# Optimization experiments

Measured on AMD Instinct MI355X. Metric: run time of the kernel, lower is better.

## Reference

```python
import jax, jax.numpy as jnp
import numpy as np

B, T, X, H, Z, G, Y = 4096, 32, 256, 256, 256, 128, 2


def _xavier(key, fan_in, fan_out):
    lim = float(np.sqrt(6.0 / (fan_in + fan_out)))
    return jax.random.uniform(key, (fan_in, fan_out), jnp.float32, -lim, lim)


def setup_inputs() -> dict:
    key = jax.random.key(0)
    ks = jax.random.split(key, 18)
    return {
        "x": jax.random.normal(ks[0], (B, T, X), jnp.float32),
        "y_ph": jax.random.uniform(ks[1], (B, T, Y), jnp.float32),
        "T_ph": jax.random.randint(ks[2], (B,), 1, T + 1),  # 1..T valid days
        "h0": jnp.tanh(jax.random.normal(ks[3], (B, H), jnp.float32)),   # tanh(randn) init state
        "z0": jnp.tanh(jax.random.normal(ks[4], (B, Z), jnp.float32)),
        "eps": jax.random.normal(ks[5], (T, B, Z), jnp.float32),          # reparam noise per step
        # gate / candidate nets: fan_in = x + h + z
        "Wr": _xavier(ks[6], X + H + Z, H), "br": jnp.zeros((H,), jnp.float32),
        "Wu": _xavier(ks[7], X + H + Z, H), "bu": jnp.zeros((H,), jnp.float32),
        "Wh": _xavier(ks[8], X + H + Z, H), "bh": jnp.zeros((H,), jnp.float32),
        # prior latent net: fan_in = x + h
        "Wzp": _xavier(ks[9], X + H, Z), "bzp": jnp.zeros((Z,), jnp.float32),
        "Wpm": _xavier(ks[10], Z, Z), "bpm": jnp.zeros((Z,), jnp.float32),
        "Wps": _xavier(ks[11], Z, Z), "bps": jnp.zeros((Z,), jnp.float32),
        # posterior latent net: fan_in = x + h + y
        "Wzq": _xavier(ks[12], X + H + Y, Z), "bzq": jnp.zeros((Z,), jnp.float32),
        "Wqm": _xavier(ks[13], Z, Z), "bqm": jnp.zeros((Z,), jnp.float32),
        "Wqs": _xavier(ks[14], Z, Z), "bqs": jnp.zeros((Z,), jnp.float32),
        # output nets
        "Wg": _xavier(ks[15], X + H + Z, G), "bg": jnp.zeros((G,), jnp.float32),
        "Wy": _xavier(ks[16], G, Y), "by": jnp.zeros((Y,), jnp.float32),
    }


def reference(x, y_ph, T_ph, h0, z0, eps,
              Wr, br, Wu, bu, Wh, bh,
              Wzp, bzp, Wpm, bpm, Wps, bps,
              Wzq, bzq, Wqm, bqm, Wqs, bqs,
              Wg, bg, Wy, by):
    x_t = jnp.transpose(x, (1, 0, 2))     # [T, B, X]
    y_t = jnp.transpose(y_ph, (1, 0, 2))  # [T, B, Y]

    def step(carry, inp):
        h_prev, z_prev = carry
        xt, yt, et = inp
        ga = jnp.concatenate([xt, h_prev, z_prev], axis=-1)
        r = jax.nn.sigmoid(ga @ Wr + br)
        u = jax.nn.sigmoid(ga @ Wu + bu)
        ha = jnp.concatenate([xt, r * h_prev, z_prev], axis=-1)
        h_tilde = jnp.tanh(ha @ Wh + bh)
        h = (1.0 - u) * h_prev + u * h_tilde
        # prior p(z_t | x_t, h_t): z_prior = mean (is_prior=True)
        hzp = jnp.tanh(jnp.concatenate([xt, h], axis=-1) @ Wzp + bzp)
        mu_p = hzp @ Wpm + bpm
        sd_p = jnp.sqrt(jnp.exp(hzp @ Wps + bps))
        z_prior = mu_p
        # posterior q(z_t | x_t, h_t, y_t): reparameterized sample
        hzq = jnp.tanh(jnp.concatenate([xt, h, yt], axis=-1) @ Wzq + bzq)
        mu_q = hzq @ Wqm + bqm
        sd_q = jnp.sqrt(jnp.exp(hzq @ Wqs + bqs))
        z_post = mu_q + sd_q * et
        # KL(q || p) for diagonal Normals
        kl = jnp.log(sd_p / sd_q) + (sd_q ** 2 + (mu_q - mu_p) ** 2) / (2.0 * sd_p ** 2) - 0.5
        return (h, z_post), (h, z_post, z_prior, kl)

    (_, _), (h_s, z_post, z_prior, kl) = jax.lax.scan(step, (h0, z0), (x_t, y_t, eps))
    h_s = jnp.transpose(h_s, (1, 0, 2))      # [B, T, H]
    z_post = jnp.transpose(z_post, (1, 0, 2))
    kl = jnp.transpose(kl, (1, 0, 2)).sum(axis=-1)  # [B, T]

    g = jnp.tanh(jnp.concatenate([x, h_s, z_post], axis=-1) @ Wg + bg)  # [B, T, G]
    y = jax.nn.softmax(g @ Wy + by, axis=-1)                             # [B, T, Y]
    g_T = g[jnp.arange(x.shape[0]), T_ph - 1]                            # [B, G] (training, daily_att)
    return (y, kl, g_T)
```

## Files before the change

### kernel.cpp

```cpp
#include <hip/hip_runtime.h>

typedef unsigned short u16;
typedef unsigned int u32;
typedef __attribute__((ext_vector_type(8))) short short8;
typedef __attribute__((ext_vector_type(4))) float float4v;
typedef __attribute__((ext_vector_type(2))) float float2v;

#define B_SZ 4096
#define T_SZ 32
#define XD 256
#define HD 256
#define ZD 256
#define GD 128
#define YD 2

#define BM 64
#define NW 16

#define W1_OFF 0
#define W2_OFF 393216
#define W3_OFF 589824
#define W4_OFF 868352
#define WG_OFF 1130496
#define WTOT   1228800

#define YTOT  (B_SZ*T_SZ*YD)
#define KLTOT (B_SZ*T_SZ)

#define UST 264

__device__ __forceinline__ u16 f2bf(float f) {
    u32 u = __float_as_uint(f);
    u32 r = (u + 0x7fffu + ((u >> 16) & 1u)) >> 16;
    return (u16)r;
}
__device__ __forceinline__ float bf2f(u16 h) {
    return __uint_as_float(((u32)h) << 16);
}
__device__ __forceinline__ float tanh_f(float x) {
    float e = __expf(2.f * x);
    return 1.f - 2.f / (e + 1.f);
}
__device__ __forceinline__ float sigm_f(float x) {
    return 1.f / (1.f + __expf(-x));
}

__device__ __forceinline__ int aga_off(int r, int k) {
    return (((r >> 4) * 24 + (k >> 5)) << 9) + ((((k >> 3) & 3) * 16 + (r & 15)) << 3) + (k & 7);
}
__device__ __forceinline__ int a3_off(int r, int k) {
    return (((r >> 4) * 8 + (k >> 5)) << 9) + ((((k >> 3) & 3) * 16 + (r & 15)) << 3) + (k & 7);
}

#define MFMA(a, b, c) __builtin_amdgcn_mfma_f32_16x16x32_bf16(a, b, c, 0, 0, 0)

__global__ void prep_weights(const float* __restrict__ Wr, const float* __restrict__ Wu,
                             const float* __restrict__ Wh, const float* __restrict__ Wzp,
                             const float* __restrict__ Wzq, const float* __restrict__ Wpm,
                             const float* __restrict__ Wps, const float* __restrict__ Wqm,
                             const float* __restrict__ Wqs, const float* __restrict__ Wg,
                             u16* __restrict__ wts)
{
    int o = blockIdx.x * 256 + threadIdx.x;
    if (o >= WTOT) return;
    int mat, w, KT;
    if (o < W2_OFF)      { mat = 0; w = o;          KT = 24; }
    else if (o < W3_OFF) { mat = 1; w = o - W2_OFF; KT = 24; }
    else if (o < W4_OFF) { mat = 2; w = o - W3_OFF; KT = 17; }
    else if (o < WG_OFF) { mat = 3; w = o - W4_OFF; KT = 8;  }
    else                 { mat = 4; w = o - WG_OFF; KT = 24; }
    int nt  = w / (KT * 512);
    int rem = w - nt * (KT * 512);
    int kt  = rem >> 9;
    int q   = rem & 511;
    int lane = q >> 3, j = q & 7;
    int n = (nt << 4) | (lane & 15);
    int k = (kt << 5) + ((lane >> 4) << 3) + j;
    float v = 0.f;
    switch (mat) {
        case 0: v = (n < 256) ? Wr[k * 256 + n] : Wu[k * 256 + (n - 256)]; break;
        case 1: v = Wh[k * 256 + n]; break;
        case 2: v = (n < 256) ? (k < 512 ? Wzp[k * 256 + n] : 0.f)
                              : (k < 514 ? Wzq[k * 256 + (n - 256)] : 0.f); break;
        case 3: { int sel = n >> 8; int nn = n & 255;
                  const float* s = (sel == 0) ? Wpm : (sel == 1) ? Wps : (sel == 2) ? Wqm : Wqs;
                  v = s[k * 256 + nn]; } break;
        default: v = Wg[k * 128 + n]; break;
    }
    wts[o] = f2bf(v);
}

__global__ __launch_bounds__(1024, 4) void vrnn_all(
    const float* __restrict__ x,   const float* __restrict__ y_ph,
    const int*   __restrict__ Tph, const float* __restrict__ h0,
    const float* __restrict__ z0,  const float* __restrict__ eps,
    const float* __restrict__ br,  const float* __restrict__ bu,
    const float* __restrict__ bh,  const float* __restrict__ bzp,
    const float* __restrict__ bpm, const float* __restrict__ bps,
    const float* __restrict__ bzq, const float* __restrict__ bqm,
    const float* __restrict__ bqs, const float* __restrict__ bg,
    const float* __restrict__ by,  const float* __restrict__ Wy,
    const u16*   __restrict__ wts, float* __restrict__ out)
{
    __shared__ __align__(16) u16   a_ga[96 * 512];
    __shared__ __align__(16) u16   a3u[16896];
    __shared__ float part[8 * BM * 2];
    __shared__ float kl_acc[BM];
    __shared__ int   tph_s[BM];

    const int tid  = threadIdx.x;
    const int wv   = tid >> 6;
    const int lane = tid & 63;
    const int quad = lane >> 4;
    const int l15  = lane & 15;
    const int b0   = blockIdx.x * BM;

    const int c10 = wv * 32 + l15;
    const float bs1_0 = (c10 < 256) ? br[c10] : bu[c10 - 256];
    const float bs1_1 = (c10 + 16 < 256) ? br[c10 + 16] : bu[c10 + 16 - 256];
    const int c2  = wv * 16 + l15;
    const float bh_r  = bh[c2];
    const float bzp_r = bzp[c2];
    const float bzq_r = bzq[c2];
    const float b4pm = bpm[c2], b4ps = bps[c2], b4qm = bqm[c2], b4qs = bqs[c2];
    const int c5  = (wv >> 1) * 16 + l15;
    const int mt5 = wv & 1;
    const float bg_r = bg[c5];
    const float wy0 = Wy[c5 * 2], wy1 = Wy[c5 * 2 + 1];
    const float by0 = by[0], by1 = by[1];

    if (tid < BM) tph_s[tid] = Tph[b0 + tid];

    float h32r[16];
#pragma unroll
    for (int m = 0; m < 4; ++m)
#pragma unroll
        for (int i = 0; i < 4; ++i) {
            int row = m * 16 + quad * 4 + i;
            h32r[m * 4 + i] = __builtin_nontemporal_load(&h0[(size_t)(b0 + row) * HD + c2]);
        }

    const int sr  = tid >> 4;
    const int scc = (tid & 15) * 16;

    float4v xn[4];
    {
        const float* xp = &x[((size_t)(b0 + sr) * T_SZ + 0) * XD + scc];
#pragma unroll
        for (int q = 0; q < 4; ++q) xn[q] = __builtin_nontemporal_load((const float4v*)(xp + q * 4));

        const float* hp = &h0[(size_t)(b0 + sr) * HD + scc];
        const float* zp = &z0[(size_t)(b0 + sr) * ZD + scc];
        float4v hv[4], zv[4];
#pragma unroll
        for (int q = 0; q < 4; ++q) {
            hv[q] = __builtin_nontemporal_load((const float4v*)(hp + q * 4));
            zv[q] = __builtin_nontemporal_load((const float4v*)(zp + q * 4));
        }
        short8 hs0, hs1, zs0, zs1;
#pragma unroll
        for (int j = 0; j < 4; ++j) {
            hs0[j] = (short)f2bf(hv[0][j]); hs0[4 + j] = (short)f2bf(hv[1][j]);
            hs1[j] = (short)f2bf(hv[2][j]); hs1[4 + j] = (short)f2bf(hv[3][j]);
            zs0[j] = (short)f2bf(zv[0][j]); zs0[4 + j] = (short)f2bf(zv[1][j]);
            zs1[j] = (short)f2bf(zv[2][j]); zs1[4 + j] = (short)f2bf(zv[3][j]);
        }
        *(short8*)&a_ga[aga_off(sr, 256 + scc)]     = hs0;
        *(short8*)&a_ga[aga_off(sr, 256 + scc + 8)] = hs1;
        *(short8*)&a_ga[aga_off(sr, 512 + scc)]     = zs0;
        *(short8*)&a_ga[aga_off(sr, 512 + scc + 8)] = zs1;
    }
    __syncthreads();

    const float4v zero4 = {0.f, 0.f, 0.f, 0.f};
    float yA0 = 0.f, yA1 = 0.f, yB0 = 0.f, yB1 = 0.f, klA = 0.f, klB = 0.f;

    for (int t = 0; t < T_SZ; ++t) {
        {
            short8 s0, s1;
#pragma unroll
            for (int j = 0; j < 4; ++j) {
                s0[j] = (short)f2bf(xn[0][j]); s0[4 + j] = (short)f2bf(xn[1][j]);
                s1[j] = (short)f2bf(xn[2][j]); s1[4 + j] = (short)f2bf(xn[3][j]);
            }
            *(short8*)&a_ga[aga_off(sr, scc)]     = s0;
            *(short8*)&a_ga[aga_off(sr, scc + 8)] = s1;
        }
        __syncthreads();

        {
            const u16* pB0 = wts + W1_OFF + (((2 * wv    ) * 24) << 9) + lane * 8;
            const u16* pB1 = wts + W1_OFF + (((2 * wv + 1) * 24) << 9) + lane * 8;
            short8 r0[2], r1[2];
            r0[0] = *(const short8*)pB0;         r1[0] = *(const short8*)pB1;
            r0[1] = *(const short8*)(pB0 + 512); r1[1] = *(const short8*)(pB1 + 512);
            float4v a0[4], a1[4];
#pragma unroll
            for (int m = 0; m < 4; ++m) { a0[m] = zero4; a1[m] = zero4; }
#pragma unroll
            for (int kt = 0; kt < 24; ++kt) {
                short8 bc0 = r0[kt & 1], bc1 = r1[kt & 1];
                if (kt + 2 < 24) {
                    r0[kt & 1] = *(const short8*)(pB0 + ((kt + 2) << 9));
                    r1[kt & 1] = *(const short8*)(pB1 + ((kt + 2) << 9));
                }
#pragma unroll
                for (int m = 0; m < 4; ++m) {
                    short8 aF = *(const short8*)&a_ga[((m * 24 + kt) << 9) + lane * 8];
                    a0[m] = MFMA(aF, bc0, a0[m]);
                    a1[m] = MFMA(aF, bc1, a1[m]);
                }
            }
            __syncthreads();
#pragma unroll
            for (int m = 0; m < 4; ++m)
#pragma unroll
                for (int i = 0; i < 4; ++i) {
                    int row = m * 16 + quad * 4 + i;
                    {
                        float v = a0[m][i];
                        if (c10 < 256) {
                            int o = aga_off(row, 256 + c10);
                            float rr = sigm_f(v + bs1_0);
                            a_ga[o] = f2bf(rr * bf2f(a_ga[o]));
                        } else {
                            a3u[row * UST + (c10 - 256)] = f2bf(sigm_f(v + bs1_0));
                        }
                    }
                    {
                        int c = c10 + 16;
                        float v = a1[m][i];
                        if (c < 256) {
                            int o = aga_off(row, 256 + c);
                            float rr = sigm_f(v + bs1_1);
                            a_ga[o] = f2bf(rr * bf2f(a_ga[o]));
                        } else {
                            a3u[row * UST + (c - 256)] = f2bf(sigm_f(v + bs1_1));
                        }
                    }
                }
            __syncthreads();
        }

        {
            const u16* pB = wts + W2_OFF + ((wv * 24) << 9) + lane * 8;
            short8 rr2[2];
            rr2[0] = *(const short8*)pB; rr2[1] = *(const short8*)(pB + 512);
            float4v a[4];
#pragma unroll
            for (int m = 0; m < 4; ++m) a[m] = zero4;
#pragma unroll
            for (int kt = 0; kt < 24; ++kt) {
                short8 bc = rr2[kt & 1];
                if (kt + 2 < 24) rr2[kt & 1] = *(const short8*)(pB + ((kt + 2) << 9));
#pragma unroll
                for (int m = 0; m < 4; ++m) {
                    short8 aF = *(const short8*)&a_ga[((m * 24 + kt) << 9) + lane * 8];
                    a[m] = MFMA(aF, bc, a[m]);
                }
            }
            __syncthreads();
#pragma unroll
            for (int m = 0; m < 4; ++m)
#pragma unroll
                for (int i = 0; i < 4; ++i) {
                    int row = m * 16 + quad * 4 + i;
                    float ht = tanh_f(a[m][i] + bh_r);
                    float uu = bf2f(a3u[row * UST + c2]);
                    float h  = (1.f - uu) * h32r[m * 4 + i] + uu * ht;
                    h32r[m * 4 + i] = h;
                    a_ga[aga_off(row, 256 + c2)] = f2bf(h);
                }
            if (tid < 256) {
                int r = tid >> 2, grp = tid & 3;
                short8 v = {0, 0, 0, 0, 0, 0, 0, 0};
                if (grp == 0) {
                    const float* yp = &y_ph[((size_t)(b0 + r) * T_SZ + t) * YD];
                    v[0] = (short)f2bf(__builtin_nontemporal_load(yp));
                    v[1] = (short)f2bf(__builtin_nontemporal_load(yp + 1));
                }
                *(short8*)&a_ga[aga_off(r, 512 + grp * 8)] = v;
            }
            __syncthreads();
        }

        {
            const u16* pB = wts + W3_OFF + ((wv * 17) << 9) + lane * 8;
            short8 r3[2];
            r3[0] = *(const short8*)pB; r3[1] = *(const short8*)(pB + 512);
            float4v a[4];
#pragma unroll
            for (int m = 0; m < 4; ++m) a[m] = zero4;
#pragma unroll
            for (int kt = 0; kt < 16; ++kt) {
                short8 bc = r3[kt & 1];
                if (kt + 2 < 16) r3[kt & 1] = *(const short8*)(pB + ((kt + 2) << 9));
#pragma unroll
                for (int m = 0; m < 4; ++m) {
                    short8 aF = *(const short8*)&a_ga[((m * 24 + kt) << 9) + lane * 8];
                    a[m] = MFMA(aF, bc, a[m]);
                }
            }
#pragma unroll
            for (int m = 0; m < 4; ++m)
#pragma unroll
                for (int i = 0; i < 4; ++i) {
                    int row = m * 16 + quad * 4 + i;
                    a3u[a3_off(row, c2)] = f2bf(tanh_f(a[m][i] + bzp_r));
                }
            __syncthreads();
        }

        float mu_p[16], s_p[16];
        {
            const u16* pBm = wts + W4_OFF + ((wv * 8) << 9) + lane * 8;
            const u16* pBs = wts + W4_OFF + (((16 + wv) * 8) << 9) + lane * 8;
            short8 rm[2], rs[2];
            rm[0] = *(const short8*)pBm;         rs[0] = *(const short8*)pBs;
            rm[1] = *(const short8*)(pBm + 512); rs[1] = *(const short8*)(pBs + 512);
            float4v am[4], as4[4];
#pragma unroll
            for (int m = 0; m < 4; ++m) { am[m] = zero4; as4[m] = zero4; }
#pragma unroll
            for (int kt = 0; kt < 8; ++kt) {
                short8 bm = rm[kt & 1], bs = rs[kt & 1];
                if (kt + 2 < 8) {
                    rm[kt & 1] = *(const short8*)(pBm + ((kt + 2) << 9));
                    rs[kt & 1] = *(const short8*)(pBs + ((kt + 2) << 9));
                }
#pragma unroll
                for (int m = 0; m < 4; ++m) {
                    short8 aF = *(const short8*)&a3u[((m * 8 + kt) << 9) + lane * 8];
                    am[m]  = MFMA(aF, bm, am[m]);
                    as4[m] = MFMA(aF, bs, as4[m]);
                }
            }
#pragma unroll
            for (int m = 0; m < 4; ++m)
#pragma unroll
                for (int i = 0; i < 4; ++i) {
                    mu_p[m * 4 + i] = am[m][i]  + b4pm;
                    s_p[m * 4 + i]  = as4[m][i] + b4ps;
                }
        }

        float er[16];
        {
#pragma unroll
            for (int m = 0; m < 4; ++m)
#pragma unroll
                for (int i = 0; i < 4; ++i) {
                    int row = m * 16 + quad * 4 + i;
                    er[m * 4 + i] = __builtin_nontemporal_load(
                        &eps[((size_t)t * B_SZ + (b0 + row)) * ZD + c2]);
                }
            const u16* pB = wts + W3_OFF + (((16 + wv) * 17) << 9) + lane * 8;
            short8 r3[2];
            r3[0] = *(const short8*)pB; r3[1] = *(const short8*)(pB + 512);
            float4v a[4];
#pragma unroll
            for (int m = 0; m < 4; ++m) a[m] = zero4;
#pragma unroll
            for (int kt = 0; kt < 17; ++kt) {
                short8 bc = r3[kt & 1];
                if (kt + 2 < 17) r3[kt & 1] = *(const short8*)(pB + ((kt + 2) << 9));
#pragma unroll
                for (int m = 0; m < 4; ++m) {
                    short8 aF = *(const short8*)&a_ga[((m * 24 + kt) << 9) + lane * 8];
                    a[m] = MFMA(aF, bc, a[m]);
                }
            }
            if (tid < BM) kl_acc[tid] = 0.f;
            __syncthreads();
#pragma unroll
            for (int m = 0; m < 4; ++m)
#pragma unroll
                for (int i = 0; i < 4; ++i) {
                    int row = m * 16 + quad * 4 + i;
                    a3u[a3_off(row, c2)] = f2bf(tanh_f(a[m][i] + bzq_r));
                }
            __syncthreads();
        }

        {
            const u16* pBm = wts + W4_OFF + (((32 + wv) * 8) << 9) + lane * 8;
            const u16* pBs = wts + W4_OFF + (((48 + wv) * 8) << 9) + lane * 8;
            short8 rm[2], rs[2];
            rm[0] = *(const short8*)pBm;         rs[0] = *(const short8*)pBs;
            rm[1] = *(const short8*)(pBm + 512); rs[1] = *(const short8*)(pBs + 512);
            float4v am[4], as4[4];
#pragma unroll
            for (int m = 0; m < 4; ++m) { am[m] = zero4; as4[m] = zero4; }
#pragma unroll
            for (int kt = 0; kt < 8; ++kt) {
                short8 bm = rm[kt & 1], bs = rs[kt & 1];
                if (kt + 2 < 8) {
                    rm[kt & 1] = *(const short8*)(pBm + ((kt + 2) << 9));
                    rs[kt & 1] = *(const short8*)(pBs + ((kt + 2) << 9));
                }
#pragma unroll
                for (int m = 0; m < 4; ++m) {
                    short8 aF = *(const short8*)&a3u[((m * 8 + kt) << 9) + lane * 8];
                    am[m]  = MFMA(aF, bm, am[m]);
                    as4[m] = MFMA(aF, bs, as4[m]);
                }
            }
            float kls[16];
#pragma unroll
            for (int m = 0; m < 4; ++m)
#pragma unroll
                for (int i = 0; i < 4; ++i) {
                    int row = m * 16 + quad * 4 + i;
                    float mq = am[m][i]  + b4qm;
                    float sq = as4[m][i] + b4qs;
                    float mp = mu_p[m * 4 + i], sp = s_p[m * 4 + i];
                    float zpost = mq + __expf(0.5f * sq) * er[m * 4 + i];
                    float dmu = mq - mp;
                    kls[m * 4 + i] = 0.5f * (sp - sq)
                                   + (__expf(sq) + dmu * dmu) * 0.5f * __expf(-sp) - 0.5f;
                    a_ga[aga_off(row, 512 + c2)] = f2bf(zpost);
                }
#pragma unroll
            for (int m = 0; m < 4; ++m)
#pragma unroll
                for (int i = 0; i < 4; ++i) {
                    float v = kls[m * 4 + i];
                    v += __shfl_xor(v, 1); v += __shfl_xor(v, 2);
                    v += __shfl_xor(v, 4); v += __shfl_xor(v, 8);
                    if (l15 == 0) atomicAdd(&kl_acc[m * 16 + quad * 4 + i], v);
                }
            __syncthreads();
            if ((tid & 15) == (t >> 1)) {
                float k = kl_acc[tid >> 4];
                if ((t & 1) == 0) klA = k; else klB = k;
            }
        }

        {
            if (t + 1 < T_SZ) {
                const float* xp = &x[((size_t)(b0 + sr) * T_SZ + (t + 1)) * XD + scc];
#pragma unroll
                for (int q = 0; q < 4; ++q)
                    xn[q] = __builtin_nontemporal_load((const float4v*)(xp + q * 4));
            }
            const u16* pB = wts + WG_OFF + (((wv >> 1) * 24) << 9) + lane * 8;
            short8 rg[2];
            rg[0] = *(const short8*)pB; rg[1] = *(const short8*)(pB + 512);
            float4v a5[2];
            a5[0] = zero4; a5[1] = zero4;
#pragma unroll
            for (int kt = 0; kt < 24; ++kt) {
                short8 bc = rg[kt & 1];
                if (kt + 2 < 24) rg[kt & 1] = *(const short8*)(pB + ((kt + 2) << 9));
                short8 aFa = *(const short8*)&a_ga[(((mt5    ) * 24 + kt) << 9) + lane * 8];
                short8 aFb = *(const short8*)&a_ga[(((mt5 + 2) * 24 + kt) << 9) + lane * 8];
                a5[0] = MFMA(aFa, bc, a5[0]);
                a5[1] = MFMA(aFb, bc, a5[1]);
            }
#pragma unroll
            for (int half = 0; half < 2; ++half) {
                int m = mt5 + 2 * half;
#pragma unroll
                for (int i = 0; i < 4; ++i) {
                    int row = m * 16 + quad * 4 + i;
                    float g = tanh_f(a5[half][i] + bg_r);
                    if (tph_s[row] - 1 == t)
                        __builtin_nontemporal_store(g,
                            &out[YTOT + KLTOT + (size_t)(b0 + row) * GD + c5]);
                    float p0 = g * wy0, p1 = g * wy1;
                    p0 += __shfl_xor(p0, 1); p0 += __shfl_xor(p0, 2);
                    p0 += __shfl_xor(p0, 4); p0 += __shfl_xor(p0, 8);
                    p1 += __shfl_xor(p1, 1); p1 += __shfl_xor(p1, 2);
                    p1 += __shfl_xor(p1, 4); p1 += __shfl_xor(p1, 8);
                    if (l15 == 0) {
                        part[((wv >> 1) * BM + row) * 2]     = p0;
                        part[((wv >> 1) * BM + row) * 2 + 1] = p1;
                    }
                }
            }
            __syncthreads();
            if ((tid & 15) == (t >> 1)) {
                int r = tid >> 4;
                float s0 = by0, s1 = by1;
#pragma unroll
                for (int j = 0; j < 8; ++j) {
                    s0 += part[(j * BM + r) * 2];
                    s1 += part[(j * BM + r) * 2 + 1];
                }
                float mx = fmaxf(s0, s1);
                float e0 = __expf(s0 - mx), e1 = __expf(s1 - mx);
                float inv = 1.f / (e0 + e1);
                if ((t & 1) == 0) { yA0 = e0 * inv; yA1 = e1 * inv; }
                else              { yB0 = e0 * inv; yB1 = e1 * inv; }
            }
        }
    }

    {
        int r = tid >> 4, tt = tid & 15;
        float4v yv = {yA0, yA1, yB0, yB1};
        __builtin_nontemporal_store(yv,
            (float4v*)&out[((size_t)(b0 + r) * T_SZ + tt * 2) * YD]);
        float2v kv = {klA, klB};
        __builtin_nontemporal_store(kv,
            (float2v*)&out[YTOT + (size_t)(b0 + r) * T_SZ + tt * 2]);
    }
}

extern "C" void kernel_launch(void* const* d_in, const int* in_sizes, int n_in,
                              void* d_out, int out_size, void* d_ws, size_t ws_size,
                              hipStream_t stream)
{
    const float* x   = (const float*)d_in[0];
    const float* yph = (const float*)d_in[1];
    const int*   Tph = (const int*)  d_in[2];
    const float* h0  = (const float*)d_in[3];
    const float* z0  = (const float*)d_in[4];
    const float* eps = (const float*)d_in[5];
    const float* Wr  = (const float*)d_in[6];
    const float* br  = (const float*)d_in[7];
    const float* Wu  = (const float*)d_in[8];
    const float* bu  = (const float*)d_in[9];
    const float* Wh  = (const float*)d_in[10];
    const float* bh  = (const float*)d_in[11];
    const float* Wzp = (const float*)d_in[12];
    const float* bzp = (const float*)d_in[13];
    const float* Wpm = (const float*)d_in[14];
    const float* bpm = (const float*)d_in[15];
    const float* Wps = (const float*)d_in[16];
    const float* bps = (const float*)d_in[17];
    const float* Wzq = (const float*)d_in[18];
    const float* bzq = (const float*)d_in[19];
    const float* Wqm = (const float*)d_in[20];
    const float* bqm = (const float*)d_in[21];
    const float* Wqs = (const float*)d_in[22];
    const float* bqs = (const float*)d_in[23];
    const float* Wg  = (const float*)d_in[24];
    const float* bg  = (const float*)d_in[25];
    const float* Wy  = (const float*)d_in[26];
    const float* by  = (const float*)d_in[27];
    u16*   wts = (u16*)d_ws;
    float* out = (float*)d_out;

    hipLaunchKernelGGL(prep_weights, dim3((WTOT + 255) / 256), dim3(256), 0, stream,
                       Wr, Wu, Wh, Wzp, Wzq, Wpm, Wps, Wqm, Wqs, Wg, wts);
    hipLaunchKernelGGL(vrnn_all, dim3(B_SZ / BM), dim3(1024), 0, stream,
                       x, yph, Tph, h0, z0, eps, br, bu, bh, bzp, bpm, bps,
                       bzq, bqm, bqs, bg, by, Wy, wts, out);
}
```

Before: 3.976 ms.

## Fuse prior and posterior latent GEMMs and process batch tile in halves

Merges the separate prior and posterior hidden-layer GEMMs into one pass that shares A-fragment LDS loads, and likewise fuses the four mean/scale GEMMs. To keep the shared a3u buffer the same size, the 64-row tile is split into two 32-row halves, each with its own barriers. The aim is fewer LDS reads of a_ga and fewer barriers per phase, and the eps loads move to just before their use. In exchange, weight fragments are re-read from global/L2 twice per step (once per half) and more registers are live at once.

New measurement: 4.662 ms. 17.3% more time.

```diff
diff --git a/kernel.cpp b/kernel.cpp
--- a/kernel.cpp
+++ b/kernel.cpp
@@ -48,8 +48,8 @@
 __device__ __forceinline__ int aga_off(int r, int k) {
     return (((r >> 4) * 24 + (k >> 5)) << 9) + ((((k >> 3) & 3) * 16 + (r & 15)) << 3) + (k & 7);
 }
-__device__ __forceinline__ int a3_off(int r, int k) {
-    return (((r >> 4) * 8 + (k >> 5)) << 9) + ((((k >> 3) & 3) * 16 + (r & 15)) << 3) + (k & 7);
+__device__ __forceinline__ int a3h_off(int r, int k, int pq) {
+    return (((pq * 2 + (r >> 4)) * 8 + (k >> 5)) << 9) + ((((k >> 3) & 3) * 16 + (r & 15)) << 3) + (k & 7);
 }
 
 #define MFMA(a, b, c) __builtin_amdgcn_mfma_f32_16x16x32_bf16(a, b, c, 0, 0, 0)
@@ -284,156 +284,104 @@
             __syncthreads();
         }
 
-        {
-            const u16* pB = wts + W3_OFF + ((wv * 17) << 9) + lane * 8;
-            short8 r3[2];
-            r3[0] = *(const short8*)pB; r3[1] = *(const short8*)(pB + 512);
-            float4v a[4];
-#pragma unroll
-            for (int m = 0; m < 4; ++m) a[m] = zero4;
-#pragma unroll
-            for (int kt = 0; kt < 16; ++kt) {
-                short8 bc = r3[kt & 1];
-                if (kt + 2 < 16) r3[kt & 1] = *(const short8*)(pB + ((kt + 2) << 9));
-#pragma unroll
-                for (int m = 0; m < 4; ++m) {
-                    short8 aF = *(const short8*)&a_ga[((m * 24 + kt) << 9) + lane * 8];
-                    a[m] = MFMA(aF, bc, a[m]);
-                }
-            }
-#pragma unroll
-            for (int m = 0; m < 4; ++m)
-#pragma unroll
-                for (int i = 0; i < 4; ++i) {
-                    int row = m * 16 + quad * 4 + i;
-                    a3u[a3_off(row, c2)] = f2bf(tanh_f(a[m][i] + bzp_r));
-                }
-            __syncthreads();
-        }
-
-        float mu_p[16], s_p[16];
-        {
-            const u16* pBm = wts + W4_OFF + ((wv * 8) << 9) + lane * 8;
-            const u16* pBs = wts + W4_OFF + (((16 + wv) * 8) << 9) + lane * 8;
-            short8 rm[2], rs[2];
-            rm[0] = *(const short8*)pBm;         rs[0] = *(const short8*)pBs;
-            rm[1] = *(const short8*)(pBm + 512); rs[1] = *(const short8*)(pBs + 512);
-            float4v am[4], as4[4];
-#pragma unroll
-            for (int m = 0; m < 4; ++m) { am[m] = zero4; as4[m] = zero4; }
-#pragma unroll
-            for (int kt = 0; kt < 8; ++kt) {
-                short8 bm = rm[kt & 1], bs = rs[kt & 1];
-                if (kt + 2 < 8) {
-                    rm[kt & 1] = *(const short8*)(pBm + ((kt + 2) << 9));
-                    rs[kt & 1] = *(const short8*)(pBs + ((kt + 2) << 9));
-                }
-#pragma unroll
-                for (int m = 0; m < 4; ++m) {
-                    short8 aF = *(const short8*)&a3u[((m * 8 + kt) << 9) + lane * 8];
-                    am[m]  = MFMA(aF, bm, am[m]);
-                    as4[m] = MFMA(aF, bs, as4[m]);
-                }
-            }
-#pragma unroll
-            for (int m = 0; m < 4; ++m)
-#pragma unroll
-                for (int i = 0; i < 4; ++i) {
-                    mu_p[m * 4 + i] = am[m][i]  + b4pm;
-                    s_p[m * 4 + i]  = as4[m][i] + b4ps;
-                }
-        }
-
-        float er[16];
-        {
-#pragma unroll
-            for (int m = 0; m < 4; ++m)
-#pragma unroll
-                for (int i = 0; i < 4; ++i) {
-                    int row = m * 16 + quad * 4 + i;
-                    er[m * 4 + i] = __builtin_nontemporal_load(
-                        &eps[((size_t)t * B_SZ + (b0 + row)) * ZD + c2]);
-                }
-            const u16* pB = wts + W3_OFF + (((16 + wv) * 17) << 9) + lane * 8;
-            short8 r3[2];
-            r3[0] = *(const short8*)pB; r3[1] = *(const short8*)(pB + 512);
-            float4v a[4];
-#pragma unroll
-            for (int m = 0; m < 4; ++m) a[m] = zero4;
-#pragma unroll
-            for (int kt = 0; kt < 17; ++kt) {
-                short8 bc = r3[kt & 1];
-                if (kt + 2 < 17) r3[kt & 1] = *(const short8*)(pB + ((kt + 2) << 9));
-#pragma unroll
-                for (int m = 0; m < 4; ++m) {
-                    short8 aF = *(const short8*)&a_ga[((m * 24 + kt) << 9) + lane * 8];
-                    a[m] = MFMA(aF, bc, a[m]);
-                }
-            }
-            if (tid < BM) kl_acc[tid] = 0.f;
-            __syncthreads();
-#pragma unroll
-            for (int m = 0; m < 4; ++m)
-#pragma unroll
-                for (int i = 0; i < 4; ++i) {
-                    int row = m * 16 + quad * 4 + i;
-                    a3u[a3_off(row, c2)] = f2bf(tanh_f(a[m][i] + bzq_r));
-                }
-            __syncthreads();
-        }
-
-        {
-            const u16* pBm = wts + W4_OFF + (((32 + wv) * 8) << 9) + lane * 8;
-            const u16* pBs = wts + W4_OFF + (((48 + wv) * 8) << 9) + lane * 8;
-            short8 rm[2], rs[2];
-            rm[0] = *(const short8*)pBm;         rs[0] = *(const short8*)pBs;
-            rm[1] = *(const short8*)(pBm + 512); rs[1] = *(const short8*)(pBs + 512);
-            float4v am[4], as4[4];
-#pragma unroll
-            for (int m = 0; m < 4; ++m) { am[m] = zero4; as4[m] = zero4; }
-#pragma unroll
-            for (int kt = 0; kt < 8; ++kt) {
-                short8 bm = rm[kt & 1], bs = rs[kt & 1];
-                if (kt + 2 < 8) {
-                    rm[kt & 1] = *(const short8*)(pBm + ((kt + 2) << 9));
-                    rs[kt & 1] = *(const short8*)(pBs + ((kt + 2) << 9));
-                }
-#pragma unroll
-                for (int m = 0; m < 4; ++m) {
-                    short8 aF = *(const short8*)&a3u[((m * 8 + kt) << 9) + lane * 8];
-                    am[m]  = MFMA(aF, bm, am[m]);
-                    as4[m] = MFMA(aF, bs, as4[m]);
-                }
-            }
-            float kls[16];
-#pragma unroll
-            for (int m = 0; m < 4; ++m)
-#pragma unroll
-                for (int i = 0; i < 4; ++i) {
-                    int row = m * 16 + quad * 4 + i;
-                    float mq = am[m][i]  + b4qm;
-                    float sq = as4[m][i] + b4qs;
-                    float mp = mu_p[m * 4 + i], sp = s_p[m * 4 + i];
-                    float zpost = mq + __expf(0.5f * sq) * er[m * 4 + i];
-                    float dmu = mq - mp;
-                    kls[m * 4 + i] = 0.5f * (sp - sq)
-                                   + (__expf(sq) + dmu * dmu) * 0.5f * __expf(-sp) - 0.5f;
-                    a_ga[aga_off(row, 512 + c2)] = f2bf(zpost);
-                }
-#pragma unroll
-            for (int m = 0; m < 4; ++m)
-#pragma unroll
-                for (int i = 0; i < 4; ++i) {
-                    float v = kls[m * 4 + i];
-                    v += __shfl_xor(v, 1); v += __shfl_xor(v, 2);
-                    v += __shfl_xor(v, 4); v += __shfl_xor(v, 8);
-                    if (l15 == 0) atomicAdd(&kl_acc[m * 16 + quad * 4 + i], v);
-                }
-            __syncthreads();
-            if ((tid & 15) == (t >> 1)) {
-                float k = kl_acc[tid >> 4];
-                if ((t & 1) == 0) klA = k; else klB = k;
-            }
+#pragma unroll
+        for (int half = 0; half < 2; ++half) {
+            {
+                const u16* pBp = wts + W3_OFF + ((wv * 17) << 9) + lane * 8;
+                const u16* pBq = wts + W3_OFF + (((16 + wv) * 17) << 9) + lane * 8;
+                short8 rp[2], rq[2];
+                rp[0] = *(const short8*)pBp; rp[1] = *(const short8*)(pBp + 512);
+                rq[0] = *(const short8*)pBq; rq[1] = *(const short8*)(pBq + 512);
+                float4v aP[2], aQ[2];
+                aP[0] = zero4; aP[1] = zero4; aQ[0] = zero4; aQ[1] = zero4;
+#pragma unroll
+                for (int kt = 0; kt < 17; ++kt) {
+                    short8 bq = rq[kt & 1];
+                    short8 bp = rp[kt & 1];
+                    if (kt + 2 < 17) rq[kt & 1] = *(const short8*)(pBq + ((kt + 2) << 9));
+                    if (kt + 2 < 16) rp[kt & 1] = *(const short8*)(pBp + ((kt + 2) << 9));
+#pragma unroll
+                    for (int m2 = 0; m2 < 2; ++m2) {
+                        short8 aF = *(const short8*)&a_ga[(((half * 2 + m2) * 24 + kt) << 9) + lane * 8];
+                        aQ[m2] = MFMA(aF, bq, aQ[m2]);
+                        if (kt < 16) aP[m2] = MFMA(aF, bp, aP[m2]);
+                    }
+                }
+                if (half == 0 && tid < BM) kl_acc[tid] = 0.f;
+#pragma unroll
+                for (int m2 = 0; m2 < 2; ++m2)
+#pragma unroll
+                    for (int i = 0; i < 4; ++i) {
+                        int r5 = m2 * 16 + quad * 4 + i;
+                        a3u[a3h_off(r5, c2, 0)] = f2bf(tanh_f(aP[m2][i] + bzp_r));
+                        a3u[a3h_off(r5, c2, 1)] = f2bf(tanh_f(aQ[m2][i] + bzq_r));
+                    }
+                __syncthreads();
+            }
+            {
+                const u16* pB0 = wts + W4_OFF + (((      wv) * 8) << 9) + lane * 8;
+                const u16* pB1 = wts + W4_OFF + (((16 + wv) * 8) << 9) + lane * 8;
+                const u16* pB2 = wts + W4_OFF + (((32 + wv) * 8) << 9) + lane * 8;
+                const u16* pB3 = wts + W4_OFF + (((48 + wv) * 8) << 9) + lane * 8;
+                float er8[8];
+#pragma unroll
+                for (int m2 = 0; m2 < 2; ++m2)
+#pragma unroll
+                    for (int i = 0; i < 4; ++i) {
+                        int row = half * 32 + m2 * 16 + quad * 4 + i;
+                        er8[m2 * 4 + i] = __builtin_nontemporal_load(
+                            &eps[((size_t)t * B_SZ + (b0 + row)) * ZD + c2]);
+                    }
+                short8 r0[2], r1[2], r2[2], r3[2];
+                r0[0] = *(const short8*)pB0;         r1[0] = *(const short8*)pB1;
+                r2[0] = *(const short8*)pB2;         r3[0] = *(const short8*)pB3;
+                r0[1] = *(const short8*)(pB0 + 512); r1[1] = *(const short8*)(pB1 + 512);
+                r2[1] = *(const short8*)(pB2 + 512); r3[1] = *(const short8*)(pB3 + 512);
+                float4v amp[2], asp[2], amq[2], asq[2];
+                amp[0] = zero4; amp[1] = zero4; asp[0] = zero4; asp[1] = zero4;
+                amq[0] = zero4; amq[1] = zero4; asq[0] = zero4; asq[1] = zero4;
+#pragma unroll
+                for (int kt = 0; kt < 8; ++kt) {
+                    short8 b0c = r0[kt & 1], b1c = r1[kt & 1];
+                    short8 b2c = r2[kt & 1], b3c = r3[kt & 1];
+                    if (kt + 2 < 8) {
+                        r0[kt & 1] = *(const short8*)(pB0 + ((kt + 2) << 9));
+                        r1[kt & 1] = *(const short8*)(pB1 + ((kt + 2) << 9));
+                        r2[kt & 1] = *(const short8*)(pB2 + ((kt + 2) << 9));
+                        r3[kt & 1] = *(const short8*)(pB3 + ((kt + 2) << 9));
+                    }
+#pragma unroll
+                    for (int m2 = 0; m2 < 2; ++m2) {
+                        short8 aP = *(const short8*)&a3u[(((m2    ) * 8 + kt) << 9) + lane * 8];
+                        short8 aQ = *(const short8*)&a3u[(((2 + m2) * 8 + kt) << 9) + lane * 8];
+                        amp[m2] = MFMA(aP, b0c, amp[m2]); asp[m2] = MFMA(aP, b1c, asp[m2]);
+                        amq[m2] = MFMA(aQ, b2c, amq[m2]); asq[m2] = MFMA(aQ, b3c, asq[m2]);
+                    }
+                }
+#pragma unroll
+                for (int m2 = 0; m2 < 2; ++m2)
+#pragma unroll
+                    for (int i = 0; i < 4; ++i) {
+                        int row = half * 32 + m2 * 16 + quad * 4 + i;
+                        float mp = amp[m2][i] + b4pm;
+                        float sp = asp[m2][i] + b4ps;
+                        float mq = amq[m2][i] + b4qm;
+                        float sq = asq[m2][i] + b4qs;
+                        float zpost = mq + __expf(0.5f * sq) * er8[m2 * 4 + i];
+                        float dmu = mq - mp;
+                        float kl = 0.5f * (sp - sq)
+                                 + (__expf(sq) + dmu * dmu) * 0.5f * __expf(-sp) - 0.5f;
+                        a_ga[aga_off(row, 512 + c2)] = f2bf(zpost);
+                        kl += __shfl_xor(kl, 1); kl += __shfl_xor(kl, 2);
+                        kl += __shfl_xor(kl, 4); kl += __shfl_xor(kl, 8);
+                        if (l15 == 0) atomicAdd(&kl_acc[row], kl);
+                    }
+                __syncthreads();
+            }
+        }
+        if ((tid & 15) == (t >> 1)) {
+            float k = kl_acc[tid >> 4];
+            if ((t & 1) == 0) klA = k; else klB = k;
         }
 
         {
```
